# Kernel optimization log

Measured on AMD Instinct MI355X. Metric: run time of the kernel, lower is better.

Reference implementation:

```python
import jax, jax.numpy as jnp
import numpy as np

U = 128            # channel (mode) size after split_mode
NUM_OUT_SEG = 16   # output segments


def setup_inputs() -> dict:
    key = jax.random.key(0)
    ks = jax.random.split(key, 16)
    B = 16384          # batch (num nodes)
    NUM_X0 = 10        # weight table rows (e.g. chemical elements)
    C = 300            # num_couplings (x0 segments)
    S = 32             # num_in_segments (x1 segments)
    P1, P2, P3 = 32, 64, 96  # paths per correlation degree 1,2,3
    inp = {
        'x0': jax.random.normal(ks[0], (NUM_X0, C * U), dtype=jnp.float32),
        'i0': jax.random.randint(ks[1], (B,), 0, NUM_X0),
        'x1': jax.random.normal(ks[2], (B, S * U), dtype=jnp.float32),
        'idx1': jax.random.randint(ks[3], (P1, 1), 0, S),
        'w1': jax.random.randint(ks[4], (P1,), 0, C),
        'o1': jax.random.randint(ks[5], (P1,), 0, NUM_OUT_SEG),
        'c1': jax.random.normal(ks[6], (P1,), dtype=jnp.float32),
        'idx2': jax.random.randint(ks[7], (P2, 2), 0, S),
        'w2': jax.random.randint(ks[8], (P2,), 0, C),
        'o2': jax.random.randint(ks[9], (P2,), 0, NUM_OUT_SEG),
        'c2': jax.random.normal(ks[10], (P2,), dtype=jnp.float32),
        'idx3': jax.random.randint(ks[11], (P3, 3), 0, S),
        'w3': jax.random.randint(ks[12], (P3,), 0, C),
        'o3': jax.random.randint(ks[13], (P3,), 0, NUM_OUT_SEG),
        'c3': jax.random.normal(ks[14], (P3,), dtype=jnp.float32),
    }
    return inp


def _symmetric_contraction(x0, i0, x1, paths):
    # x0: (num_x0, C*U) weight table, i0: (B,) gather index, x1: (B, S*U)
    B = x1.shape[0]
    g0 = x0.reshape(x0.shape[0], -1, U)[i0]   # (B, C, U) indexed gather
    x1r = x1.reshape(B, -1, U)                # (B, S, U)
    out = jnp.zeros((NUM_OUT_SEG, B, U), dtype=x1.dtype)
    for idx, w, o, c in paths:
        # path product: coeff * x0[i0][w_p] * prod_k x1[idx_{p,k}]
        t = g0[:, w] * c[None, :, None]       # (B, P, U)
        for k in range(idx.shape[1]):          # degree <= 3 (static)
            t = t * x1r[:, idx[:, k]]
        # scatter-add over output segments
        out = out + jax.ops.segment_sum(t.transpose(1, 0, 2), o,
                                        num_segments=NUM_OUT_SEG)
    return out.transpose(1, 0, 2).reshape(B, NUM_OUT_SEG * U)


def reference(x0, i0, x1, idx1, w1, o1, c1, idx2, w2, o2, c2,
              idx3, w3, o3, c3):
    paths = ((idx1, w1, o1, c1), (idx2, w2, o2, c2), (idx3, w3, o3, c3))
    return _symmetric_contraction(x0, i0, x1, paths)
```

## Files before the change

kernel.cpp:

```cpp
#include <hip/hip_runtime.h>
#include <hip/hip_bf16.h>

#define U_DIM 128
#define NUM_OUT_SEG 16
#define C_DIM 300
#define S_DIM 32
#define NUM_X0 10
#define P1 32
#define P2 64
#define P3 96
#define P_TOT (P1 + P2 + P3)

typedef float vfloat4 __attribute__((ext_vector_type(4)));

__global__ void prep_kernel(const int* __restrict__ idx1, const int* __restrict__ w1,
                            const int* __restrict__ o1, const float* __restrict__ c1,
                            const int* __restrict__ idx2, const int* __restrict__ w2,
                            const int* __restrict__ o2, const float* __restrict__ c2,
                            const int* __restrict__ idx3, const int* __restrict__ w3,
                            const int* __restrict__ o3, const float* __restrict__ c3,
                            int* __restrict__ soff, int4* __restrict__ meta) {
    __shared__ int cnt[48];
    __shared__ int off[49];
    __shared__ int cur[48];
    int t = threadIdx.x;
    if (t < 48) cnt[t] = 0;
    __syncthreads();

    int key = -1, w = 0, packed = 0;
    float c = 0.f;
    if (t < P_TOT) {
        int deg, o, a0 = 0, a1 = 0, a2 = 0;
        if (t < P1) {
            int p = t;
            deg = 1; w = w1[p]; o = o1[p]; c = c1[p];
            a0 = idx1[p];
        } else if (t < P1 + P2) {
            int p = t - P1;
            deg = 2; w = w2[p]; o = o2[p]; c = c2[p];
            a0 = idx2[2 * p]; a1 = idx2[2 * p + 1];
        } else {
            int p = t - P1 - P2;
            deg = 3; w = w3[p]; o = o3[p]; c = c3[p];
            a0 = idx3[3 * p]; a1 = idx3[3 * p + 1]; a2 = idx3[3 * p + 2];
        }
        key = o * 3 + (deg - 1);
        packed = a0 | (a1 << 8) | (a2 << 16);
        atomicAdd(&cnt[key], 1);
    }
    __syncthreads();
    if (t == 0) {
        int a = 0;
        for (int k = 0; k < 48; ++k) { off[k] = a; a += cnt[k]; }
        off[48] = a;
    }
    __syncthreads();
    if (t < 49) soff[t] = off[t];
    if (t < 48) cur[t] = off[t];
    __syncthreads();
    if (t < P_TOT) {
        int r = atomicAdd(&cur[key], 1);
        meta[r] = make_int4(w, packed, __float_as_int(c), 0);
    }
}

__global__ __launch_bounds__(256, 4) void contract_kernel(
    const float* __restrict__ x0, const int* __restrict__ i0,
    const float* __restrict__ x1, const int* __restrict__ soff,
    const int4* __restrict__ meta, float* __restrict__ out) {
    __shared__ vfloat4 x1s[S_DIM * 32];

    const int tid = threadIdx.x;
    const int g = tid >> 5;
    const int u4 = tid & 31;
    const long b = blockIdx.x;

    const vfloat4* x1p = (const vfloat4*)(x1 + b * (S_DIM * U_DIM));
#pragma unroll
    for (int k = 0; k < 4; ++k) {
        x1s[k * 256 + tid] = x1p[k * 256 + tid];
    }

    const vfloat4* g0 = (const vfloat4*)x0 + (long)i0[b] * (C_DIM * 32);
    vfloat4* outb = (vfloat4*)(out + b * (NUM_OUT_SEG * U_DIM));
    __syncthreads();

#pragma unroll
    for (int oo = 0; oo < 2; ++oo) {
        const int o = g * 2 + oo;
        vfloat4 acc = (vfloat4)(0.f);
        int p = soff[o * 3];
        const int e1 = soff[o * 3 + 1];
        const int e2 = soff[o * 3 + 2];
        const int e3 = soff[o * 3 + 3];

        for (; p < e1; ++p) {
            int4 m = meta[p];
            float cc = __int_as_float(m.z);
            vfloat4 gg = g0[(m.x << 5) + u4];
            vfloat4 xa = x1s[((m.y & 255) << 5) + u4];
            acc += (cc * gg) * xa;
        }
#pragma unroll 2
        for (; p < e2; ++p) {
            int4 m = meta[p];
            float cc = __int_as_float(m.z);
            vfloat4 gg = g0[(m.x << 5) + u4];
            vfloat4 xa = x1s[((m.y & 255) << 5) + u4];
            vfloat4 xb = x1s[(((m.y >> 8) & 255) << 5) + u4];
            acc += (cc * gg) * (xa * xb);
        }
#pragma unroll 2
        for (; p < e3; ++p) {
            int4 m = meta[p];
            float cc = __int_as_float(m.z);
            vfloat4 gg = g0[(m.x << 5) + u4];
            vfloat4 xa = x1s[((m.y & 255) << 5) + u4];
            vfloat4 xb = x1s[(((m.y >> 8) & 255) << 5) + u4];
            vfloat4 xc = x1s[(((m.y >> 16) & 255) << 5) + u4];
            acc += (cc * gg) * (xa * xb * xc);
        }
        __builtin_nontemporal_store(acc, &outb[o * 32 + u4]);
    }
}

extern "C" void kernel_launch(void* const* d_in, const int* in_sizes, int n_in,
                              void* d_out, int out_size, void* d_ws, size_t ws_size,
                              hipStream_t stream) {
    const float* x0 = (const float*)d_in[0];
    const int* i0 = (const int*)d_in[1];
    const float* x1 = (const float*)d_in[2];
    const int* idx1 = (const int*)d_in[3];
    const int* w1 = (const int*)d_in[4];
    const int* o1 = (const int*)d_in[5];
    const float* c1 = (const float*)d_in[6];
    const int* idx2 = (const int*)d_in[7];
    const int* w2 = (const int*)d_in[8];
    const int* o2 = (const int*)d_in[9];
    const float* c2 = (const float*)d_in[10];
    const int* idx3 = (const int*)d_in[11];
    const int* w3 = (const int*)d_in[12];
    const int* o3 = (const int*)d_in[13];
    const float* c3 = (const float*)d_in[14];

    int* soff = (int*)d_ws;
    int4* meta = (int4*)((char*)d_ws + 256);

    const int B = in_sizes[1];

    prep_kernel<<<1, 256, 0, stream>>>(idx1, w1, o1, c1, idx2, w2, o2, c2,
                                       idx3, w3, o3, c3, soff, meta);
    contract_kernel<<<B, 256, 0, stream>>>(x0, i0, x1, soff, meta, (float*)d_out);
}
```

Before: 505.0 us.

## Unify path degrees via ones row and pad segments for 4-way unrolled scalar-metadata loop

Pads every path to degree 3 using an extra all-ones row in shared memory, so each output segment runs one loop instead of three. Segments are padded to multiples of four with zero-coefficient entries, allowing a 4-way unrolled loop that reads metadata through readfirstlane into scalar registers. The block grows to 512 threads with 64 lanes of float2 per wave. The cost is extra wasted multiplies and LDS reads for lower-degree and padding paths, and narrower per-lane loads.

```diff
diff --git a/kernel.cpp b/kernel.cpp
--- a/kernel.cpp
+++ b/kernel.cpp
@@ -10,8 +10,10 @@
 #define P2 64
 #define P3 96
 #define P_TOT (P1 + P2 + P3)
+#define ONES_ROW 32
+#define META_CAP 256
 
-typedef float vfloat4 __attribute__((ext_vector_type(4)));
+typedef float vfloat2 __attribute__((ext_vector_type(2)));
 
 __global__ void prep_kernel(const int* __restrict__ idx1, const int* __restrict__ w1,
                             const int* __restrict__ o1, const float* __restrict__ c1,
@@ -20,43 +22,46 @@
                             const int* __restrict__ idx3, const int* __restrict__ w3,
                             const int* __restrict__ o3, const float* __restrict__ c3,
                             int* __restrict__ soff, int4* __restrict__ meta) {
-    __shared__ int cnt[48];
-    __shared__ int off[49];
-    __shared__ int cur[48];
-    int t = threadIdx.x;
-    if (t < 48) cnt[t] = 0;
+    __shared__ int cnt[NUM_OUT_SEG];
+    __shared__ int off[NUM_OUT_SEG + 1];
+    __shared__ int cur[NUM_OUT_SEG];
+    const int t = threadIdx.x;
+    if (t < NUM_OUT_SEG) cnt[t] = 0;
+    meta[t] = make_int4(0, ONES_ROW | (ONES_ROW << 8) | (ONES_ROW << 16), 0, 0);
     __syncthreads();
 
     int key = -1, w = 0, packed = 0;
     float c = 0.f;
     if (t < P_TOT) {
-        int deg, o, a0 = 0, a1 = 0, a2 = 0;
+        int a0, a1 = ONES_ROW, a2 = ONES_ROW;
         if (t < P1) {
             int p = t;
-            deg = 1; w = w1[p]; o = o1[p]; c = c1[p];
+            w = w1[p]; key = o1[p]; c = c1[p];
             a0 = idx1[p];
         } else if (t < P1 + P2) {
             int p = t - P1;
-            deg = 2; w = w2[p]; o = o2[p]; c = c2[p];
+            w = w2[p]; key = o2[p]; c = c2[p];
             a0 = idx2[2 * p]; a1 = idx2[2 * p + 1];
         } else {
             int p = t - P1 - P2;
-            deg = 3; w = w3[p]; o = o3[p]; c = c3[p];
+            w = w3[p]; key = o3[p]; c = c3[p];
             a0 = idx3[3 * p]; a1 = idx3[3 * p + 1]; a2 = idx3[3 * p + 2];
         }
-        key = o * 3 + (deg - 1);
         packed = a0 | (a1 << 8) | (a2 << 16);
         atomicAdd(&cnt[key], 1);
     }
     __syncthreads();
     if (t == 0) {
         int a = 0;
-        for (int k = 0; k < 48; ++k) { off[k] = a; a += cnt[k]; }
-        off[48] = a;
+        for (int k = 0; k < NUM_OUT_SEG; ++k) {
+            off[k] = a;
+            a += (cnt[k] + 3) & ~3;
+        }
+        off[NUM_OUT_SEG] = a;
     }
     __syncthreads();
-    if (t < 49) soff[t] = off[t];
-    if (t < 48) cur[t] = off[t];
+    if (t < NUM_OUT_SEG + 1) soff[t] = off[t];
+    if (t < NUM_OUT_SEG) cur[t] = off[t];
     __syncthreads();
     if (t < P_TOT) {
         int r = atomicAdd(&cur[key], 1);
@@ -64,63 +69,77 @@
     }
 }
 
-__global__ __launch_bounds__(256, 4) void contract_kernel(
+__global__ __launch_bounds__(512, 8) void contract_kernel(
     const float* __restrict__ x0, const int* __restrict__ i0,
     const float* __restrict__ x1, const int* __restrict__ soff,
     const int4* __restrict__ meta, float* __restrict__ out) {
-    __shared__ vfloat4 x1s[S_DIM * 32];
+    __shared__ vfloat2 x1s[(S_DIM + 1) * 64];
 
     const int tid = threadIdx.x;
-    const int g = tid >> 5;
-    const int u4 = tid & 31;
+    const int wave = tid >> 6;
+    const int lane = tid & 63;
     const long b = blockIdx.x;
 
-    const vfloat4* x1p = (const vfloat4*)(x1 + b * (S_DIM * U_DIM));
+    const vfloat2* x1p = (const vfloat2*)(x1 + b * (S_DIM * U_DIM));
 #pragma unroll
     for (int k = 0; k < 4; ++k) {
-        x1s[k * 256 + tid] = x1p[k * 256 + tid];
+        x1s[k * 512 + tid] = x1p[k * 512 + tid];
     }
+    if (tid < 64) x1s[S_DIM * 64 + tid] = (vfloat2)(1.0f);
 
-    const vfloat4* g0 = (const vfloat4*)x0 + (long)i0[b] * (C_DIM * 32);
-    vfloat4* outb = (vfloat4*)(out + b * (NUM_OUT_SEG * U_DIM));
+    const vfloat2* gbase = (const vfloat2*)x0 + (long)i0[b] * (C_DIM * 64);
+    vfloat2* outb = (vfloat2*)(out + b * (NUM_OUT_SEG * U_DIM));
     __syncthreads();
 
-#pragma unroll
+#pragma unroll 1
     for (int oo = 0; oo < 2; ++oo) {
-        const int o = g * 2 + oo;
-        vfloat4 acc = (vfloat4)(0.f);
-        int p = soff[o * 3];
-        const int e1 = soff[o * 3 + 1];
-        const int e2 = soff[o * 3 + 2];
-        const int e3 = soff[o * 3 + 3];
+        const int o = wave * 2 + oo;
+        vfloat2 acc = (vfloat2)(0.f);
+        int p = soff[o];
+        const int e = soff[o + 1];
+#pragma unroll 1
+        for (; p < e; p += 4) {
+            int4 m0 = meta[p];
+            int4 m1 = meta[p + 1];
+            int4 m2 = meta[p + 2];
+            int4 m3 = meta[p + 3];
+            const int w0 = __builtin_amdgcn_readfirstlane(m0.x) << 6;
+            const int y0 = __builtin_amdgcn_readfirstlane(m0.y);
+            const float f0 = __uint_as_float((unsigned)__builtin_amdgcn_readfirstlane(m0.z));
+            const int w1_ = __builtin_amdgcn_readfirstlane(m1.x) << 6;
+            const int y1 = __builtin_amdgcn_readfirstlane(m1.y);
+            const float f1 = __uint_as_float((unsigned)__builtin_amdgcn_readfirstlane(m1.z));
+            const int w2_ = __builtin_amdgcn_readfirstlane(m2.x) << 6;
+            const int y2 = __builtin_amdgcn_readfirstlane(m2.y);
+            const float f2 = __uint_as_float((unsigned)__builtin_amdgcn_readfirstlane(m2.z));
+            const int w3_ = __builtin_amdgcn_readfirstlane(m3.x) << 6;
+            const int y3 = __builtin_amdgcn_readfirstlane(m3.y);
+            const float f3 = __uint_as_float((unsigned)__builtin_amdgcn_readfirstlane(m3.z));
 
-        for (; p < e1; ++p) {
-            int4 m = meta[p];
-            float cc = __int_as_float(m.z);
-            vfloat4 gg = g0[(m.x << 5) + u4];
-            vfloat4 xa = x1s[((m.y & 255) << 5) + u4];
-            acc += (cc * gg) * xa;
+            vfloat2 ga = gbase[w0 + lane];
+            vfloat2 gb = gbase[w1_ + lane];
+            vfloat2 gc = gbase[w2_ + lane];
+            vfloat2 gd = gbase[w3_ + lane];
+
+            vfloat2 xa0 = x1s[((y0 & 255) << 6) + lane];
+            vfloat2 xb0 = x1s[(((y0 >> 8) & 255) << 6) + lane];
+            vfloat2 xc0 = x1s[(((y0 >> 16) & 255) << 6) + lane];
+            vfloat2 xa1 = x1s[((y1 & 255) << 6) + lane];
+            vfloat2 xb1 = x1s[(((y1 >> 8) & 255) << 6) + lane];
+            vfloat2 xc1 = x1s[(((y1 >> 16) & 255) << 6) + lane];
+            vfloat2 xa2 = x1s[((y2 & 255) << 6) + lane];
+            vfloat2 xb2 = x1s[(((y2 >> 8) & 255) << 6) + lane];
+            vfloat2 xc2 = x1s[(((y2 >> 16) & 255) << 6) + lane];
+            vfloat2 xa3 = x1s[((y3 & 255) << 6) + lane];
+            vfloat2 xb3 = x1s[(((y3 >> 8) & 255) << 6) + lane];
+            vfloat2 xc3 = x1s[(((y3 >> 16) & 255) << 6) + lane];
+
+            acc += (f0 * ga) * (xa0 * xb0 * xc0);
+            acc += (f1 * gb) * (xa1 * xb1 * xc1);
+            acc += (f2 * gc) * (xa2 * xb2 * xc2);
+            acc += (f3 * gd) * (xa3 * xb3 * xc3);
         }
-#pragma unroll 2
-        for (; p < e2; ++p) {
-            int4 m = meta[p];
-            float cc = __int_as_float(m.z);
-            vfloat4 gg = g0[(m.x << 5) + u4];
-            vfloat4 xa = x1s[((m.y & 255) << 5) + u4];
-            vfloat4 xb = x1s[(((m.y >> 8) & 255) << 5) + u4];
-            acc += (cc * gg) * (xa * xb);
-        }
-#pragma unroll 2
-        for (; p < e3; ++p) {
-            int4 m = meta[p];
-            float cc = __int_as_float(m.z);
-            vfloat4 gg = g0[(m.x << 5) + u4];
-            vfloat4 xa = x1s[((m.y & 255) << 5) + u4];
-            vfloat4 xb = x1s[(((m.y >> 8) & 255) << 5) + u4];
-            vfloat4 xc = x1s[(((m.y >> 16) & 255) << 5) + u4];
-            acc += (cc * gg) * (xa * xb * xc);
-        }
-        __builtin_nontemporal_store(acc, &outb[o * 32 + u4]);
+        __builtin_nontemporal_store(acc, &outb[o * 64 + lane]);
     }
 }
 
@@ -148,7 +167,7 @@
 
     const int B = in_sizes[1];
 
-    prep_kernel<<<1, 256, 0, stream>>>(idx1, w1, o1, c1, idx2, w2, o2, c2,
-                                       idx3, w3, o3, c3, soff, meta);
-    contract_kernel<<<B, 256, 0, stream>>>(x0, i0, x1, soff, meta, (float*)d_out);
+    prep_kernel<<<1, META_CAP, 0, stream>>>(idx1, w1, o1, c1, idx2, w2, o2, c2,
+                                            idx3, w3, o3, c3, soff, meta);
+    contract_kernel<<<B, 512, 0, stream>>>(x0, i0, x1, soff, meta, (float*)d_out);
 }
```

After: 605.6 us. 1.2x slower.

## Process two batch rows per 1024-thread block with metadata staged in LDS

Applied to the files above, without the earlier changes.

Each block now handles two batch rows with 1024 threads, where each wave owns one output segment and each half-wave owns one row, instead of 256 threads looping over two segments each. Path metadata is packed into int2 (weight index plus x1 indices in one word, coefficient in the other) and copied into shared memory, which replaces the per-iteration global int4 loads. This removes the serial two-segment loop per thread and cuts the metadata load width. In exchange it assumes B is even and uses larger blocks, which may limit scheduling flexibility. Load imbalance between waves also remains, since different output segments have different path counts.

```diff
diff --git a/kernel.cpp b/kernel.cpp
--- a/kernel.cpp
+++ b/kernel.cpp
@@ -19,18 +19,18 @@
                             const int* __restrict__ o2, const float* __restrict__ c2,
                             const int* __restrict__ idx3, const int* __restrict__ w3,
                             const int* __restrict__ o3, const float* __restrict__ c3,
-                            int* __restrict__ soff, int4* __restrict__ meta) {
+                            int* __restrict__ soff, int2* __restrict__ meta) {
     __shared__ int cnt[48];
     __shared__ int off[49];
     __shared__ int cur[48];
-    int t = threadIdx.x;
+    const int t = threadIdx.x;
     if (t < 48) cnt[t] = 0;
     __syncthreads();
 
-    int key = -1, w = 0, packed = 0;
+    int key = -1, packed = 0;
     float c = 0.f;
     if (t < P_TOT) {
-        int deg, o, a0 = 0, a1 = 0, a2 = 0;
+        int deg, o, w, a0 = 0, a1 = 0, a2 = 0;
         if (t < P1) {
             int p = t;
             deg = 1; w = w1[p]; o = o1[p]; c = c1[p];
@@ -45,7 +45,7 @@
             a0 = idx3[3 * p]; a1 = idx3[3 * p + 1]; a2 = idx3[3 * p + 2];
         }
         key = o * 3 + (deg - 1);
-        packed = a0 | (a1 << 8) | (a2 << 16);
+        packed = w | (a0 << 9) | (a1 << 14) | (a2 << 19);
         atomicAdd(&cnt[key], 1);
     }
     __syncthreads();
@@ -60,68 +60,71 @@
     __syncthreads();
     if (t < P_TOT) {
         int r = atomicAdd(&cur[key], 1);
-        meta[r] = make_int4(w, packed, __float_as_int(c), 0);
+        meta[r] = make_int2(packed, __float_as_int(c));
     }
 }
 
-__global__ __launch_bounds__(256, 4) void contract_kernel(
+__global__ __launch_bounds__(1024, 8) void contract_kernel(
     const float* __restrict__ x0, const int* __restrict__ i0,
     const float* __restrict__ x1, const int* __restrict__ soff,
-    const int4* __restrict__ meta, float* __restrict__ out) {
-    __shared__ vfloat4 x1s[S_DIM * 32];
+    const int2* __restrict__ gmeta, float* __restrict__ out) {
+    __shared__ vfloat4 x1s[2 * S_DIM * 32];
+    __shared__ int2 smeta[P_TOT];
 
     const int tid = threadIdx.x;
-    const int g = tid >> 5;
-    const int u4 = tid & 31;
-    const long b = blockIdx.x;
+    const int wave = tid >> 6;
+    const int lane = tid & 63;
+    const int h = lane >> 5;
+    const int ch = lane & 31;
+    const long b0 = (long)blockIdx.x * 2;
 
-    const vfloat4* x1p = (const vfloat4*)(x1 + b * (S_DIM * U_DIM));
-#pragma unroll
-    for (int k = 0; k < 4; ++k) {
-        x1s[k * 256 + tid] = x1p[k * 256 + tid];
+    const vfloat4* x1p = (const vfloat4*)(x1 + b0 * (S_DIM * U_DIM));
+    x1s[tid] = x1p[tid];
+    x1s[tid + 1024] = x1p[tid + 1024];
+    if (tid < P_TOT) smeta[tid] = gmeta[tid];
+
+    const int elem = i0[b0 + h];
+    const vfloat4* gseg = (const vfloat4*)x0 + (long)elem * (C_DIM * 32) + ch;
+    const vfloat4* myx1 = x1s + h * (S_DIM * 32) + ch;
+
+    int p = soff[wave * 3];
+    const int e1 = soff[wave * 3 + 1];
+    const int e2 = soff[wave * 3 + 2];
+    const int e3 = soff[wave * 3 + 3];
+    __syncthreads();
+
+    vfloat4 acc = (vfloat4)(0.f);
+
+#pragma unroll 2
+    for (; p < e1; ++p) {
+        int2 m = smeta[p];
+        float cc = __int_as_float(m.y);
+        vfloat4 g = gseg[(m.x & 0x1FF) * 32];
+        vfloat4 xa = myx1[((m.x >> 9) & 31) * 32];
+        acc += (cc * g) * xa;
+    }
+#pragma unroll 2
+    for (; p < e2; ++p) {
+        int2 m = smeta[p];
+        float cc = __int_as_float(m.y);
+        vfloat4 g = gseg[(m.x & 0x1FF) * 32];
+        vfloat4 xa = myx1[((m.x >> 9) & 31) * 32];
+        vfloat4 xb = myx1[((m.x >> 14) & 31) * 32];
+        acc += (cc * g) * (xa * xb);
+    }
+#pragma unroll 2
+    for (; p < e3; ++p) {
+        int2 m = smeta[p];
+        float cc = __int_as_float(m.y);
+        vfloat4 g = gseg[(m.x & 0x1FF) * 32];
+        vfloat4 xa = myx1[((m.x >> 9) & 31) * 32];
+        vfloat4 xb = myx1[((m.x >> 14) & 31) * 32];
+        vfloat4 xc = myx1[((m.x >> 19) & 31) * 32];
+        acc += (cc * g) * (xa * xb * xc);
     }
 
-    const vfloat4* g0 = (const vfloat4*)x0 + (long)i0[b] * (C_DIM * 32);
-    vfloat4* outb = (vfloat4*)(out + b * (NUM_OUT_SEG * U_DIM));
-    __syncthreads();
-
-#pragma unroll
-    for (int oo = 0; oo < 2; ++oo) {
-        const int o = g * 2 + oo;
-        vfloat4 acc = (vfloat4)(0.f);
-        int p = soff[o * 3];
-        const int e1 = soff[o * 3 + 1];
-        const int e2 = soff[o * 3 + 2];
-        const int e3 = soff[o * 3 + 3];
-
-        for (; p < e1; ++p) {
-            int4 m = meta[p];
-            float cc = __int_as_float(m.z);
-            vfloat4 gg = g0[(m.x << 5) + u4];
-            vfloat4 xa = x1s[((m.y & 255) << 5) + u4];
-            acc += (cc * gg) * xa;
-        }
-#pragma unroll 2
-        for (; p < e2; ++p) {
-            int4 m = meta[p];
-            float cc = __int_as_float(m.z);
-            vfloat4 gg = g0[(m.x << 5) + u4];
-            vfloat4 xa = x1s[((m.y & 255) << 5) + u4];
-            vfloat4 xb = x1s[(((m.y >> 8) & 255) << 5) + u4];
-            acc += (cc * gg) * (xa * xb);
-        }
-#pragma unroll 2
-        for (; p < e3; ++p) {
-            int4 m = meta[p];
-            float cc = __int_as_float(m.z);
-            vfloat4 gg = g0[(m.x << 5) + u4];
-            vfloat4 xa = x1s[((m.y & 255) << 5) + u4];
-            vfloat4 xb = x1s[(((m.y >> 8) & 255) << 5) + u4];
-            vfloat4 xc = x1s[(((m.y >> 16) & 255) << 5) + u4];
-            acc += (cc * gg) * (xa * xb * xc);
-        }
-        __builtin_nontemporal_store(acc, &outb[o * 32 + u4]);
-    }
+    vfloat4* outp = (vfloat4*)(out + (b0 + h) * (NUM_OUT_SEG * U_DIM)) + wave * 32 + ch;
+    __builtin_nontemporal_store(acc, outp);
 }
 
 extern "C" void kernel_launch(void* const* d_in, const int* in_sizes, int n_in,
@@ -144,11 +147,11 @@
     const float* c3 = (const float*)d_in[14];
 
     int* soff = (int*)d_ws;
-    int4* meta = (int4*)((char*)d_ws + 256);
+    int2* meta = (int2*)((char*)d_ws + 256);
 
     const int B = in_sizes[1];
 
     prep_kernel<<<1, 256, 0, stream>>>(idx1, w1, o1, c1, idx2, w2, o2, c2,
                                        idx3, w3, o3, c3, soff, meta);
-    contract_kernel<<<B, 256, 0, stream>>>(x0, i0, x1, soff, meta, (float*)d_out);
+    contract_kernel<<<B / 2, 1024, 0, stream>>>(x0, i0, x1, soff, meta, (float*)d_out);
 }
```

After: 437.0 us. -13.5%, faster.
